# Performance work log

Hardware: AMD Instinct MI355X
Metric: run time of the kernel (lower is better)

The kernel has to match this reference:

```python
import jax, jax.numpy as jnp
import numpy as np

EPS_NORM = 1e-6
EPS_Q = 1e-5


def rmsnorm(x, g):
    var = jnp.mean(jnp.square(x), axis=-1, keepdims=True)
    return x * jax.lax.rsqrt(var + EPS_NORM) * g


def act_quant(x):
    # per-token int8 absmax fake-quant (BitNet)
    scale = 127.0 / jnp.clip(jnp.max(jnp.abs(x), axis=-1, keepdims=True), EPS_Q, None)
    return jnp.clip(jnp.round(x * scale), -128.0, 127.0) / scale


def weight_quant(w):
    # per-tensor ternary (b1.58) fake-quant
    scale = 1.0 / jnp.clip(jnp.mean(jnp.abs(w)), EPS_Q, None)
    return jnp.clip(jnp.round(w * scale), -1.0, 1.0) / scale


def ste(x, fn):
    return x + jax.lax.stop_gradient(fn(x) - x)


def bitlinear(x, w, g):
    # RMSNorm -> act fake-quant (STE) -> ternary weight fake-quant (STE) -> matmul
    xn = rmsnorm(x, g)
    xq = ste(xn, act_quant)
    wq = ste(w, weight_quant)
    return jnp.einsum('bsd,od->bso', xq, wq)


def setup_inputs() -> dict:
    key = jax.random.key(0)
    k1, k2, k3 = jax.random.split(key, 3)
    B, S, D, I = 4, 4096, 2048, 5632
    x = jax.random.normal(k1, (B, S, D), dtype=jnp.float32)
    w_gate = jax.random.normal(k2, (2 * I, D), dtype=jnp.float32) * (D ** -0.5)
    g_gate = jnp.ones((D,), dtype=jnp.float32)
    w_down = jax.random.normal(k3, (D, I), dtype=jnp.float32) * (I ** -0.5)
    g_down = jnp.ones((I,), dtype=jnp.float32)
    return {"x": x, "w_gate": w_gate, "g_gate": g_gate,
            "w_down": w_down, "g_down": g_down}


def reference(x, w_gate, g_gate, w_down, g_down):
    y = bitlinear(x, w_gate, g_gate)            # [B, S, 2*I]
    gate, v = jnp.split(y, 2, axis=-1)          # chunk(2, -1)
    swiglu_out = gate * jax.nn.sigmoid(gate) * v  # swish(gate) * v
    z = bitlinear(swiglu_out, w_down, g_down)   # [B, S, D]
    return z
```

## Files before the change

kernel.cpp:

```cpp
#include <hip/hip_runtime.h>
#include <hip/hip_bf16.h>

typedef int v4i __attribute__((ext_vector_type(4)));

#define DEV __device__ __forceinline__

DEV void gload16(const void* g, void* l){
  __builtin_amdgcn_global_load_lds((const __attribute__((address_space(1))) unsigned int*)g,
                                   (__attribute__((address_space(3))) unsigned int*)l, 16, 0, 0);
}

DEV float block_sum256(float v, float* red){
#pragma unroll
  for (int o=32;o>0;o>>=1) v += __shfl_down(v,o);
  int w = threadIdx.x>>6;
  if ((threadIdx.x&63)==0) red[w]=v;
  __syncthreads();
  v = red[0]+red[1]+red[2]+red[3];
  __syncthreads();
  return v;
}
DEV float block_max256(float v, float* red){
#pragma unroll
  for (int o=32;o>0;o>>=1) v = fmaxf(v,__shfl_down(v,o));
  int w = threadIdx.x>>6;
  if ((threadIdx.x&63)==0) red[w]=v;
  __syncthreads();
  v = fmaxf(fmaxf(red[0],red[1]),fmaxf(red[2],red[3]));
  __syncthreads();
  return v;
}

__global__ __launch_bounds__(256) void reduce_abs_kernel(const float* __restrict__ w, long n4,
                                                         float* __restrict__ partials){
  __shared__ float red[4];
  const float4* w4 = (const float4*)w;
  float s = 0.f;
  for (long i = (long)blockIdx.x*256 + threadIdx.x; i < n4; i += (long)gridDim.x*256){
    float4 v = w4[i];
    s += fabsf(v.x)+fabsf(v.y)+fabsf(v.z)+fabsf(v.w);
  }
  s = block_sum256(s, red);
  if (threadIdx.x==0) partials[blockIdx.x]=s;
}

__global__ __launch_bounds__(256) void finalize_scales_kernel(const float* __restrict__ partials,
                                                              float* __restrict__ hdr){
  __shared__ float red[4];
  float s1=0.f, s2=0.f;
  for (int i=threadIdx.x;i<1024;i+=256){ s1+=partials[i]; s2+=partials[i+1024]; }
  s1 = block_sum256(s1, red);
  s2 = block_sum256(s2, red);
  if (threadIdx.x==0){
    float m1 = s1 / 23068672.0f;
    float sc1 = 1.0f / fmaxf(m1, 1e-5f);
    hdr[0]=sc1; hdr[1]=1.0f/sc1;
    float m2 = s2 / 11534336.0f;
    float sc2 = 1.0f / fmaxf(m2, 1e-5f);
    hdr[2]=sc2; hdr[3]=1.0f/sc2;
  }
}

__global__ __launch_bounds__(256) void quant_w_kernel(const float* __restrict__ w,
                                                      signed char* __restrict__ wq, long n4,
                                                      const float* __restrict__ hdr, int hi){
  float scale = hdr[hi];
  const float4* w4 = (const float4*)w;
  unsigned* o4 = (unsigned*)wq;
  for (long i = (long)blockIdx.x*256 + threadIdx.x; i < n4; i += (long)gridDim.x*256){
    float4 v = w4[i];
    int q0 = (int)fminf(fmaxf(rintf(v.x*scale),-1.f),1.f);
    int q1 = (int)fminf(fmaxf(rintf(v.y*scale),-1.f),1.f);
    int q2 = (int)fminf(fmaxf(rintf(v.z*scale),-1.f),1.f);
    int q3 = (int)fminf(fmaxf(rintf(v.w*scale),-1.f),1.f);
    unsigned pk = (q0&0xff) | ((q1&0xff)<<8) | ((q2&0xff)<<16) | ((q3&0xff)<<24);
    o4[i] = pk;
  }
}

__global__ __launch_bounds__(256) void rms_quant_x_kernel(const float* __restrict__ x,
                                                          const float* __restrict__ g,
                                                          signed char* __restrict__ xq,
                                                          float* __restrict__ isx){
  __shared__ float red[4];
  const int row = blockIdx.x, t = threadIdx.x;
  const float* xr = x + (size_t)row*2048 + t*8;
  float4 a = *(const float4*)xr;
  float4 b = *(const float4*)(xr+4);
  float xv[8] = {a.x,a.y,a.z,a.w,b.x,b.y,b.z,b.w};
  float ss = 0.f;
#pragma unroll
  for (int i=0;i<8;i++) ss += xv[i]*xv[i];
  ss = block_sum256(ss, red);
  float rs = rsqrtf(ss*(1.0f/2048.0f) + 1e-6f);
  const float* gr = g + t*8;
  float4 ga = *(const float4*)gr;
  float4 gb = *(const float4*)(gr+4);
  float gv[8] = {ga.x,ga.y,ga.z,ga.w,gb.x,gb.y,gb.z,gb.w};
  float xn[8]; float m = 0.f;
#pragma unroll
  for (int i=0;i<8;i++){ xn[i] = xv[i]*rs*gv[i]; m = fmaxf(m, fabsf(xn[i])); }
  m = block_max256(m, red);
  float scale = 127.0f / fmaxf(m, 1e-5f);
  unsigned long long pk = 0;
#pragma unroll
  for (int i=0;i<8;i++){
    int q = (int)fminf(fmaxf(rintf(xn[i]*scale), -128.0f), 127.0f);
    pk |= (unsigned long long)(unsigned char)(signed char)q << (8*i);
  }
  *(unsigned long long*)(xq + (size_t)row*2048 + t*8) = pk;
  if (t==0) isx[row] = 1.0f/scale;
}

__global__ __launch_bounds__(256) void rms_quant_sg_kernel(const __hip_bfloat16* __restrict__ sg,
                                                           const float* __restrict__ g,
                                                           signed char* __restrict__ xq,
                                                           float* __restrict__ isx){
  __shared__ float red[4];
  const int row = blockIdx.x, t = threadIdx.x;
  const unsigned* sr = (const unsigned*)(sg + (size_t)row*5632);
  float s[22];
  float ss = 0.f;
#pragma unroll
  for (int i=0;i<11;i++){
    unsigned u = sr[t + i*256];
    float f0 = __uint_as_float(u<<16);
    float f1 = __uint_as_float(u & 0xffff0000u);
    s[2*i]=f0; s[2*i+1]=f1;
    ss += f0*f0 + f1*f1;
  }
  ss = block_sum256(ss, red);
  float rs = rsqrtf(ss*(1.0f/5632.0f) + 1e-6f);
  const float2* g2 = (const float2*)g;
  float xn[22]; float m = 0.f;
#pragma unroll
  for (int i=0;i<11;i++){
    float2 gv = g2[t + i*256];
    xn[2*i]   = s[2*i]  *rs*gv.x;
    xn[2*i+1] = s[2*i+1]*rs*gv.y;
    m = fmaxf(m, fmaxf(fabsf(xn[2*i]), fabsf(xn[2*i+1])));
  }
  m = block_max256(m, red);
  float scale = 127.0f / fmaxf(m, 1e-5f);
  short* o2 = (short*)(xq + (size_t)row*5632);
#pragma unroll
  for (int i=0;i<11;i++){
    int q0 = (int)fminf(fmaxf(rintf(xn[2*i]  *scale), -128.0f), 127.0f);
    int q1 = (int)fminf(fmaxf(rintf(xn[2*i+1]*scale), -128.0f), 127.0f);
    o2[t + i*256] = (short)((q0 & 0xff) | ((q1 & 0xff) << 8));
  }
  if (t==0) isx[row] = 1.0f/scale;
}

__global__ __launch_bounds__(512) void gemm1_swiglu_kernel(const signed char* __restrict__ A,
                                                           const signed char* __restrict__ B,
                                                           const float* __restrict__ inv_sx,
                                                           const float* __restrict__ hdr,
                                                           __hip_bfloat16* __restrict__ out){
  constexpr int K = 2048;
  constexpr int NI = 5632;
  constexpr int NT = 32;
  __shared__ __align__(16) unsigned char smem[65536];

  const int t = threadIdx.x;
  const int lid = blockIdx.x + blockIdx.y * gridDim.x;
  const int xc = lid & 7;
  const int sx = lid >> 3;
  const int ch = sx >> 5;
  const int ii = sx & 31;
  const int bm0 = (xc*8 + (ii>>2)) * 256;
  const int bc0 = (ch*4 + (ii&3)) * 128;
  const int w = t >> 6, l = t & 63;
  const int ts = w >> 2;
  const int wv = w & 3;
  const int wr = wv * 64;
  const int hw = wv >> 1;
  const int lr = l & 15, lg = l >> 4;

  const float inv_sw = hdr[1];

  const signed char* aSrc[2]; int aOff[2];
#pragma unroll
  for (int i=0;i<2;i++){
    int c = t + i*512, r = c>>2, kp = c&3;
    aSrc[i] = A + (size_t)(bm0 + r)*K + ((kp ^ ((r>>1)&3))*16);
    aOff[i] = c*16;
  }
  const signed char* bSrc[2]; int bOff[2];
#pragma unroll
  for (int i=0;i<2;i++){
    int c = t + i*512, r = c>>2, kp = c&3;
    int grow = ((r>>7) ? NI : 0) + bc0 + (r&127);
    bSrc[i] = B + (size_t)grow*K + ((kp ^ ((r>>1)&3))*16);
    bOff[i] = 16384 + c*16;
  }
  int aoff[4];
#pragma unroll
  for (int i=0;i<4;i++){ int row = wr + i*16 + lr; aoff[i] = row*64 + ((lg ^ ((row>>1)&3))*16); }
  int boff[8];
#pragma unroll
  for (int j=0;j<8;j++){ int row = ts*128 + j*16 + lr; boff[j] = 16384 + row*64 + ((lg ^ ((row>>1)&3))*16); }

  v4i acc[4][8] = {};

#define STAGE1(BUF, KT) { unsigned char* _b = smem + (BUF)*32768;      \
    gload16(aSrc[0] + (KT)*64, _b + aOff[0]);                          \
    gload16(aSrc[1] + (KT)*64, _b + aOff[1]);                          \
    gload16(bSrc[0] + (KT)*64, _b + bOff[0]);                          \
    gload16(bSrc[1] + (KT)*64, _b + bOff[1]); }

#define COMP1(BUF) {                                                   \
  const signed char* _bs = (const signed char*)smem + (BUF)*32768;     \
  v4i af[4], bf[8];                                                    \
  _Pragma("unroll") for (int _i=0;_i<4;_i++) af[_i] = *(const v4i*)(_bs + aoff[_i]); \
  _Pragma("unroll") for (int _j=0;_j<8;_j++) bf[_j] = *(const v4i*)(_bs + boff[_j]); \
  __builtin_amdgcn_s_setprio(1);                                       \
  _Pragma("unroll") for (int _j=0;_j<8;_j++)                           \
    _Pragma("unroll") for (int _i=0;_i<4;_i++)                         \
      acc[_i][_j] = __builtin_amdgcn_mfma_i32_16x16x64_i8(af[_i], bf[_j], acc[_i][_j], 0, 0, 0); \
  __builtin_amdgcn_s_setprio(0);                                       \
}

  STAGE1(0,0); STAGE1(1,1);

  for (int kt = 0; kt < NT; ++kt){
    if (kt < NT-1) { asm volatile("s_waitcnt vmcnt(4)" ::: "memory"); }
    else           { asm volatile("s_waitcnt vmcnt(0)" ::: "memory"); }
    __builtin_amdgcn_s_barrier();
    __builtin_amdgcn_sched_barrier(0);
    COMP1(kt&1);
    __builtin_amdgcn_sched_barrier(0);
    __builtin_amdgcn_s_barrier();
    if (kt < NT-2) STAGE1(kt&1, kt+2);
  }

  float* vex = (float*)smem;
#pragma unroll
  for (int h=0; h<2; ++h){
    __syncthreads();
    if (ts == 1 && hw == h){
#pragma unroll
      for (int i=0;i<4;i++){
#pragma unroll
        for (int r=0;r<4;r++){
          int lrow = wr + i*16 + lg*4 + r;
          int lloc = lrow - h*128;
          float f = inv_sx[bm0 + lrow] * inv_sw;
#pragma unroll
          for (int j=0;j<8;j++)
            vex[lloc*128 + j*16 + lr] = (float)acc[i][j][r] * f;
        }
      }
    }
    __syncthreads();
    if (ts == 0 && hw == h){
#pragma unroll
      for (int i=0;i<4;i++){
#pragma unroll
        for (int r=0;r<4;r++){
          int lrow = wr + i*16 + lg*4 + r;
          int lloc = lrow - h*128;
          float f = inv_sx[bm0 + lrow] * inv_sw;
#pragma unroll
          for (int j=0;j<8;j++){
            float gv = (float)acc[i][j][r] * f;
            float vv = vex[lloc*128 + j*16 + lr];
            float sw = gv / (1.0f + expf(-gv)) * vv;
            acc[i][j][r] = __float_as_int(sw);
          }
        }
      }
    }
  }
  __syncthreads();
  __hip_bfloat16* obuf = (__hip_bfloat16*)smem;
  if (ts == 0){
#pragma unroll
    for (int i=0;i<4;i++){
#pragma unroll
      for (int r=0;r<4;r++){
        int lrow = wr + i*16 + lg*4 + r;
#pragma unroll
        for (int j=0;j<8;j++)
          obuf[lrow*128 + j*16 + lr] = __float2bfloat16(__int_as_float(acc[i][j][r]));
      }
    }
  }
  __syncthreads();
#pragma unroll
  for (int it=0; it<8; ++it){
    int idx = t + it*512;
    int row = idx >> 4, c16 = idx & 15;
    *(int4*)((char*)(out + (size_t)(bm0+row)*NI + bc0) + c16*16) =
        *(const int4*)((const char*)obuf + row*256 + c16*16);
  }
#undef STAGE1
#undef COMP1
}

__global__ __launch_bounds__(256) void gemm2_kernel(const signed char* __restrict__ A,
                                                    const signed char* __restrict__ B,
                                                    const float* __restrict__ inv_sx,
                                                    const float* __restrict__ hdr,
                                                    float* __restrict__ out){
  constexpr int K = 5632;
  constexpr int N = 2048;
  constexpr int NT = 44;
  __shared__ __align__(16) unsigned char smem[65536];

  const int t = threadIdx.x;
  const int lid = blockIdx.x + blockIdx.y * gridDim.x;
  const int xc = lid & 7;
  const int sx = lid >> 3;
  const int ch = sx >> 4, ii = sx & 15;
  const int bm0 = (xc*16 + (ch>>2)*4 + (ii>>2)) * 128;
  const int bn0 = ((ch&3)*4 + (ii&3)) * 128;
  const int w = t >> 6, l = t & 63;
  const int wr = (w >> 1) * 64, wc = (w & 1) * 64;
  const int lr = l & 15, lg = l >> 4;

  const float inv_sw = hdr[3];

  const signed char *aSrc[4], *bSrc[4]; int aOff[4], bOff[4];
#pragma unroll
  for (int i=0;i<4;i++){
    int cc = t + i*256; int r = cc>>3, k = cc&7;
    aSrc[i] = A + (size_t)(bm0 + r)*K + ((k ^ (r&7))*16);
    bSrc[i] = B + (size_t)(bn0 + r)*K + ((k ^ (r&7))*16);
    aOff[i] = cc*16;
    bOff[i] = 16384 + cc*16;
  }

  v4i acc[4][4] = {};

#define STAGE2(BUF, KT) do{ unsigned char* _bb = smem + (BUF)*32768;              \
  _Pragma("unroll") for (int _i=0;_i<4;_i++){                                     \
    gload16(aSrc[_i] + (KT)*128, _bb + aOff[_i]);                                 \
    gload16(bSrc[_i] + (KT)*128, _bb + bOff[_i]); } }while(0)

#define COMP2(BUF) do{                                                            \
  const signed char* _As = (const signed char*)smem + (BUF)*32768;                \
  const signed char* _Bs = _As + 16384;                                           \
  _Pragma("unroll") for (int kk=0;kk<2;++kk){                                     \
    v4i af[4], bf[4];                                                             \
    _Pragma("unroll") for (int i=0;i<4;i++){                                      \
      int row = wr + i*16 + lr;                                                   \
      af[i] = *(const v4i*)(_As + row*128 + (((kk*4+lg) ^ (row&7))*16));          \
    }                                                                             \
    _Pragma("unroll") for (int j=0;j<4;j++){                                      \
      int row = wc + j*16 + lr;                                                   \
      bf[j] = *(const v4i*)(_Bs + row*128 + (((kk*4+lg) ^ (row&7))*16));          \
    }                                                                             \
    __builtin_amdgcn_s_setprio(1);                                                \
    _Pragma("unroll") for (int i=0;i<4;i++)                                       \
      _Pragma("unroll") for (int j=0;j<4;j++)                                     \
        acc[i][j] = __builtin_amdgcn_mfma_i32_16x16x64_i8(af[i], bf[j], acc[i][j], 0, 0, 0); \
    __builtin_amdgcn_s_setprio(0);                                                \
  } }while(0)

  STAGE2(0, 0);
  STAGE2(1, 1);
  for (int kt = 0; kt < NT-2; kt += 2){
    asm volatile("s_waitcnt vmcnt(8)" ::: "memory");
    __builtin_amdgcn_s_barrier();
    __builtin_amdgcn_sched_barrier(0);
    COMP2(0);
    __builtin_amdgcn_sched_barrier(0);
    __builtin_amdgcn_s_barrier();
    STAGE2(0, kt+2);
    asm volatile("s_waitcnt vmcnt(8)" ::: "memory");
    __builtin_amdgcn_s_barrier();
    __builtin_amdgcn_sched_barrier(0);
    COMP2(1);
    __builtin_amdgcn_sched_barrier(0);
    __builtin_amdgcn_s_barrier();
    STAGE2(1, kt+3);
  }
  asm volatile("s_waitcnt vmcnt(8)" ::: "memory");
  __builtin_amdgcn_s_barrier();
  __builtin_amdgcn_sched_barrier(0);
  COMP2(0);
  __builtin_amdgcn_sched_barrier(0);
  __builtin_amdgcn_s_barrier();
  asm volatile("s_waitcnt vmcnt(0)" ::: "memory");
  __builtin_amdgcn_s_barrier();
  __builtin_amdgcn_sched_barrier(0);
  COMP2(1);
  __builtin_amdgcn_sched_barrier(0);

#pragma unroll
  for (int i=0;i<4;i++){
#pragma unroll
    for (int r=0;r<4;r++){
      int lrow = wr + i*16 + lg*4 + r;
      float f = inv_sx[bm0 + lrow] * inv_sw;
      size_t o = (size_t)(bm0 + lrow) * N + bn0;
#pragma unroll
      for (int j=0;j<4;j++)
        out[o + wc + j*16 + lr] = (float)acc[i][j][r] * f;
    }
  }
#undef STAGE2
#undef COMP2
}

extern "C" void kernel_launch(void* const* d_in, const int* in_sizes, int n_in,
                              void* d_out, int out_size, void* d_ws, size_t ws_size,
                              hipStream_t stream) {
  const float* x      = (const float*)d_in[0];
  const float* w_gate = (const float*)d_in[1];
  const float* g_gate = (const float*)d_in[2];
  const float* w_down = (const float*)d_in[3];
  const float* g_down = (const float*)d_in[4];
  float* out = (float*)d_out;

  char* p = (char*)d_ws;
  float* hdr      = (float*)p;
  float* partials = (float*)(p + 64);
  size_t off = 8448;
  signed char* wqg = (signed char*)(p + off); off += 23068672;
  signed char* wqd = (signed char*)(p + off); off += 11534336;
  signed char* xq1 = (signed char*)(p + off); off += 33554432;
  signed char* xq2 = (signed char*)(p + off); off += 92274688;
  float* isx1 = (float*)(p + off); off += 65536;
  float* isx2 = (float*)(p + off); off += 65536;
  __hip_bfloat16* sg = (__hip_bfloat16*)(p + off); off += 184549376;

  reduce_abs_kernel<<<1024,256,0,stream>>>(w_gate, 23068672/4, partials);
  reduce_abs_kernel<<<1024,256,0,stream>>>(w_down, 11534336/4, partials+1024);
  finalize_scales_kernel<<<1,256,0,stream>>>(partials, hdr);
  quant_w_kernel<<<2048,256,0,stream>>>(w_gate, wqg, 23068672/4, hdr, 0);
  quant_w_kernel<<<1024,256,0,stream>>>(w_down, wqd, 11534336/4, hdr, 2);
  rms_quant_x_kernel<<<16384,256,0,stream>>>(x, g_gate, xq1, isx1);
  gemm1_swiglu_kernel<<<dim3(44,64),512,0,stream>>>(xq1, wqg, isx1, hdr, sg);
  rms_quant_sg_kernel<<<16384,256,0,stream>>>(sg, g_down, xq2, isx2);
  gemm2_kernel<<<dim3(16,128),256,0,stream>>>(xq2, wqd, isx2, hdr, out);
}
```

Baseline: 947.4 us.

## Restructure SwiGLU GEMM1 to 256 threads with 128x128 warp tiles and BK=128

The fused gate/value int8 GEMM moves from 512 threads (8 waves, 64x128 warp tiles, BK=64) to 256 threads (4 waves, 128x128 warp tiles, BK=128), with a 128 KB double-buffered LDS and an 8-way XOR swizzle. Each wave now owns a full gate or value column block, so the SwiGLU epilogue needs one LDS exchange instead of two halves. The deeper K step and larger per-wave tile raise MFMA work per LDS read and halve the loop iterations. The cost is 256 int32 accumulators per thread, which raises register pressure and cuts occupancy, and a pipeline that waits on vmcnt(0) every iteration, which limits overlap of loads and compute.

```diff
diff --git a/kernel.cpp b/kernel.cpp
--- a/kernel.cpp
+++ b/kernel.cpp
@@ -152,15 +152,15 @@
   if (t==0) isx[row] = 1.0f/scale;
 }
 
-__global__ __launch_bounds__(512) void gemm1_swiglu_kernel(const signed char* __restrict__ A,
+__global__ __launch_bounds__(256) void gemm1_swiglu_kernel(const signed char* __restrict__ A,
                                                            const signed char* __restrict__ B,
                                                            const float* __restrict__ inv_sx,
                                                            const float* __restrict__ hdr,
                                                            __hip_bfloat16* __restrict__ out){
   constexpr int K = 2048;
   constexpr int NI = 5632;
-  constexpr int NT = 32;
-  __shared__ __align__(16) unsigned char smem[65536];
+  constexpr int NT = 16;
+  __shared__ __align__(16) unsigned char smem[131072];
 
   const int t = threadIdx.x;
   const int lid = blockIdx.x + blockIdx.y * gridDim.x;
@@ -171,131 +171,125 @@
   const int bm0 = (xc*8 + (ii>>2)) * 256;
   const int bc0 = (ch*4 + (ii&3)) * 128;
   const int w = t >> 6, l = t & 63;
-  const int ts = w >> 2;
-  const int wv = w & 3;
-  const int wr = wv * 64;
-  const int hw = wv >> 1;
+  const int rh = w >> 1;
+  const int cv = w & 1;
+  const int wr = rh * 128;
   const int lr = l & 15, lg = l >> 4;
 
   const float inv_sw = hdr[1];
 
-  const signed char* aSrc[2]; int aOff[2];
-#pragma unroll
-  for (int i=0;i<2;i++){
-    int c = t + i*512, r = c>>2, kp = c&3;
-    aSrc[i] = A + (size_t)(bm0 + r)*K + ((kp ^ ((r>>1)&3))*16);
-    aOff[i] = c*16;
-  }
-  const signed char* bSrc[2]; int bOff[2];
-#pragma unroll
-  for (int i=0;i<2;i++){
-    int c = t + i*512, r = c>>2, kp = c&3;
-    int grow = ((r>>7) ? NI : 0) + bc0 + (r&127);
-    bSrc[i] = B + (size_t)grow*K + ((kp ^ ((r>>1)&3))*16);
-    bOff[i] = 16384 + c*16;
-  }
-  int aoff[4];
-#pragma unroll
-  for (int i=0;i<4;i++){ int row = wr + i*16 + lr; aoff[i] = row*64 + ((lg ^ ((row>>1)&3))*16); }
-  int boff[8];
-#pragma unroll
-  for (int j=0;j<8;j++){ int row = ts*128 + j*16 + lr; boff[j] = 16384 + row*64 + ((lg ^ ((row>>1)&3))*16); }
-
-  v4i acc[4][8] = {};
-
-#define STAGE1(BUF, KT) { unsigned char* _b = smem + (BUF)*32768;      \
-    gload16(aSrc[0] + (KT)*64, _b + aOff[0]);                          \
-    gload16(aSrc[1] + (KT)*64, _b + aOff[1]);                          \
-    gload16(bSrc[0] + (KT)*64, _b + bOff[0]);                          \
-    gload16(bSrc[1] + (KT)*64, _b + bOff[1]); }
-
-#define COMP1(BUF) {                                                   \
-  const signed char* _bs = (const signed char*)smem + (BUF)*32768;     \
-  v4i af[4], bf[8];                                                    \
-  _Pragma("unroll") for (int _i=0;_i<4;_i++) af[_i] = *(const v4i*)(_bs + aoff[_i]); \
-  _Pragma("unroll") for (int _j=0;_j<8;_j++) bf[_j] = *(const v4i*)(_bs + boff[_j]); \
-  __builtin_amdgcn_s_setprio(1);                                       \
-  _Pragma("unroll") for (int _j=0;_j<8;_j++)                           \
-    _Pragma("unroll") for (int _i=0;_i<4;_i++)                         \
-      acc[_i][_j] = __builtin_amdgcn_mfma_i32_16x16x64_i8(af[_i], bf[_j], acc[_i][_j], 0, 0, 0); \
-  __builtin_amdgcn_s_setprio(0);                                       \
-}
-
-  STAGE1(0,0); STAGE1(1,1);
+  const int r0 = t >> 3, k0 = t & 7;
+  const signed char* aSrcB = A + (size_t)(bm0 + r0)*K + ((k0 ^ (r0&7))*16);
+  const signed char* bSrcG = B + (size_t)(bc0 + r0)*K + ((k0 ^ (r0&7))*16);
+  const signed char* bSrcV = B + (size_t)(NI + bc0 + r0)*K + ((k0 ^ (r0&7))*16);
+
+  int aoff0[8], aoff1[8], boff0[8], boff1[8];
+#pragma unroll
+  for (int i=0;i<8;i++){
+    int row = wr + i*16 + lr;
+    aoff0[i] = row*128 + ((lg ^ (row&7))*16);
+    aoff1[i] = row*128 + (((4+lg) ^ (row&7))*16);
+    int brow = cv*128 + i*16 + lr;
+    boff0[i] = 32768 + brow*128 + ((lg ^ (brow&7))*16);
+    boff1[i] = 32768 + brow*128 + (((4+lg) ^ (brow&7))*16);
+  }
+
+  v4i acc[8][8] = {};
+
+#define STAGE1(BUF, KT) { unsigned char* _b = smem + (BUF)*65536;                        \
+  _Pragma("unroll") for (int _i=0;_i<8;_i++)                                             \
+    gload16(aSrcB + (size_t)_i*32*K + (KT)*128, _b + t*16 + _i*4096);                    \
+  _Pragma("unroll") for (int _i=0;_i<4;_i++)                                             \
+    gload16(bSrcG + (size_t)_i*32*K + (KT)*128, _b + 32768 + t*16 + _i*4096);            \
+  _Pragma("unroll") for (int _i=0;_i<4;_i++)                                             \
+    gload16(bSrcV + (size_t)_i*32*K + (KT)*128, _b + 49152 + t*16 + _i*4096); }
+
+  STAGE1(0, 0);
 
   for (int kt = 0; kt < NT; ++kt){
-    if (kt < NT-1) { asm volatile("s_waitcnt vmcnt(4)" ::: "memory"); }
-    else           { asm volatile("s_waitcnt vmcnt(0)" ::: "memory"); }
+    asm volatile("s_waitcnt vmcnt(0)" ::: "memory");
     __builtin_amdgcn_s_barrier();
-    __builtin_amdgcn_sched_barrier(0);
-    COMP1(kt&1);
-    __builtin_amdgcn_sched_barrier(0);
-    __builtin_amdgcn_s_barrier();
-    if (kt < NT-2) STAGE1(kt&1, kt+2);
-  }
-
+    if (kt < NT-1) STAGE1((kt+1)&1, kt+1);
+    const signed char* bs = (const signed char*)smem + (kt&1)*65536;
+    v4i a0[8], b0[8], a1[8], b1[8];
+#pragma unroll
+    for (int i=0;i<8;i++) a0[i] = *(const v4i*)(bs + aoff0[i]);
+#pragma unroll
+    for (int j=0;j<8;j++) b0[j] = *(const v4i*)(bs + boff0[j]);
+#pragma unroll
+    for (int i=0;i<8;i++) a1[i] = *(const v4i*)(bs + aoff1[i]);
+#pragma unroll
+    for (int j=0;j<8;j++) b1[j] = *(const v4i*)(bs + boff1[j]);
+    __builtin_amdgcn_s_setprio(1);
+#pragma unroll
+    for (int j=0;j<8;j++)
+#pragma unroll
+      for (int i=0;i<8;i++)
+        acc[i][j] = __builtin_amdgcn_mfma_i32_16x16x64_i8(a0[i], b0[j], acc[i][j], 0, 0, 0);
+#pragma unroll
+    for (int j=0;j<8;j++)
+#pragma unroll
+      for (int i=0;i<8;i++)
+        acc[i][j] = __builtin_amdgcn_mfma_i32_16x16x64_i8(a1[i], b1[j], acc[i][j], 0, 0, 0);
+    __builtin_amdgcn_s_setprio(0);
+  }
+
+  __syncthreads();
   float* vex = (float*)smem;
-#pragma unroll
-  for (int h=0; h<2; ++h){
-    __syncthreads();
-    if (ts == 1 && hw == h){
-#pragma unroll
-      for (int i=0;i<4;i++){
-#pragma unroll
-        for (int r=0;r<4;r++){
-          int lrow = wr + i*16 + lg*4 + r;
-          int lloc = lrow - h*128;
-          float f = inv_sx[bm0 + lrow] * inv_sw;
-#pragma unroll
-          for (int j=0;j<8;j++)
-            vex[lloc*128 + j*16 + lr] = (float)acc[i][j][r] * f;
+  if (cv == 1){
+#pragma unroll
+    for (int i=0;i<8;i++){
+#pragma unroll
+      for (int r_=0;r_<4;r_++){
+        int lrow = wr + i*16 + lg*4 + r_;
+        float f = inv_sx[bm0 + lrow] * inv_sw;
+#pragma unroll
+        for (int j=0;j<8;j++)
+          vex[lrow*128 + j*16 + lr] = (float)acc[i][j][r_] * f;
+      }
+    }
+  }
+  __syncthreads();
+  if (cv == 0){
+#pragma unroll
+    for (int i=0;i<8;i++){
+#pragma unroll
+      for (int r_=0;r_<4;r_++){
+        int lrow = wr + i*16 + lg*4 + r_;
+        float f = inv_sx[bm0 + lrow] * inv_sw;
+#pragma unroll
+        for (int j=0;j<8;j++){
+          float gv = (float)acc[i][j][r_] * f;
+          float vv = vex[lrow*128 + j*16 + lr];
+          float sw = gv / (1.0f + expf(-gv)) * vv;
+          acc[i][j][r_] = __float_as_int(sw);
         }
       }
     }
-    __syncthreads();
-    if (ts == 0 && hw == h){
-#pragma unroll
-      for (int i=0;i<4;i++){
-#pragma unroll
-        for (int r=0;r<4;r++){
-          int lrow = wr + i*16 + lg*4 + r;
-          int lloc = lrow - h*128;
-          float f = inv_sx[bm0 + lrow] * inv_sw;
-#pragma unroll
-          for (int j=0;j<8;j++){
-            float gv = (float)acc[i][j][r] * f;
-            float vv = vex[lloc*128 + j*16 + lr];
-            float sw = gv / (1.0f + expf(-gv)) * vv;
-            acc[i][j][r] = __float_as_int(sw);
-          }
-        }
+  }
+  __syncthreads();
+  __hip_bfloat16* obuf = (__hip_bfloat16*)smem;
+  if (cv == 0){
+#pragma unroll
+    for (int i=0;i<8;i++){
+#pragma unroll
+      for (int r_=0;r_<4;r_++){
+        int lrow = wr + i*16 + lg*4 + r_;
+#pragma unroll
+        for (int j=0;j<8;j++)
+          obuf[lrow*128 + j*16 + lr] = __float2bfloat16(__int_as_float(acc[i][j][r_]));
       }
     }
   }
   __syncthreads();
-  __hip_bfloat16* obuf = (__hip_bfloat16*)smem;
-  if (ts == 0){
-#pragma unroll
-    for (int i=0;i<4;i++){
-#pragma unroll
-      for (int r=0;r<4;r++){
-        int lrow = wr + i*16 + lg*4 + r;
-#pragma unroll
-        for (int j=0;j<8;j++)
-          obuf[lrow*128 + j*16 + lr] = __float2bfloat16(__int_as_float(acc[i][j][r]));
-      }
-    }
-  }
-  __syncthreads();
-#pragma unroll
-  for (int it=0; it<8; ++it){
-    int idx = t + it*512;
+#pragma unroll
+  for (int it=0; it<16; ++it){
+    int idx = t + it*256;
     int row = idx >> 4, c16 = idx & 15;
     *(int4*)((char*)(out + (size_t)(bm0+row)*NI + bc0) + c16*16) =
         *(const int4*)((const char*)obuf + row*256 + c16*16);
   }
 #undef STAGE1
-#undef COMP1
 }
 
 __global__ __launch_bounds__(256) void gemm2_kernel(const signed char* __restrict__ A,
@@ -432,7 +426,7 @@
   quant_w_kernel<<<2048,256,0,stream>>>(w_gate, wqg, 23068672/4, hdr, 0);
   quant_w_kernel<<<1024,256,0,stream>>>(w_down, wqd, 11534336/4, hdr, 2);
   rms_quant_x_kernel<<<16384,256,0,stream>>>(x, g_gate, xq1, isx1);
-  gemm1_swiglu_kernel<<<dim3(44,64),512,0,stream>>>(xq1, wqg, isx1, hdr, sg);
+  gemm1_swiglu_kernel<<<dim3(44,64),256,0,stream>>>(xq1, wqg, isx1, hdr, sg);
   rms_quant_sg_kernel<<<16384,256,0,stream>>>(sg, g_down, xq2, isx2);
   gemm2_kernel<<<dim3(16,128),256,0,stream>>>(xq2, wqd, isx2, hdr, out);
 }
```

New measurement: 1.536 ms. 62.1% more time.
